# Performance work log

Measured on AMD Instinct MI355X. Metric: run time of the kernel, lower is better.

## Reference

```python
import jax, jax.numpy as jnp
import numpy as np

N_AGENTS = 32
UNIT_DIM = 32
STATE_DIM = 1200
N_HEAD = 8
EMBED = 64
KEY_HID = 2 * EMBED
HYPER = 256
V_HID = 4 * EMBED
ATTEND_REG_COEF = 0.001
BS, T = 128, 32


def setup_inputs() -> dict:
    key = jax.random.key(0)
    ks = jax.random.split(key, 12)
    def lin(k, shape, fan_in):
        return jax.random.normal(k, shape, jnp.float32) / np.sqrt(fan_in)
    return dict(
        agent_qs=jax.random.normal(ks[0], (BS, T, N_AGENTS), jnp.float32),
        states=jax.random.normal(ks[1], (BS, T, STATE_DIM), jnp.float32),
        actions=jax.random.randint(ks[2], (BS, T, N_AGENTS), 0, 20),
        sel_W1=lin(ks[3], (N_HEAD, HYPER, STATE_DIM), STATE_DIM),
        sel_b1=jnp.zeros((N_HEAD, HYPER), jnp.float32),
        sel_W2=lin(ks[4], (N_HEAD, EMBED, HYPER), HYPER),
        key_W1=lin(ks[5], (N_HEAD, KEY_HID, UNIT_DIM + 1), UNIT_DIM + 1),
        key_b1=jnp.zeros((N_HEAD, KEY_HID), jnp.float32),
        key_W2=lin(ks[6], (N_HEAD, EMBED, KEY_HID), KEY_HID),
        wh_W1=lin(ks[7], (HYPER, STATE_DIM), STATE_DIM),
        wh_b1=jnp.zeros((HYPER,), jnp.float32),
        wh_W2=lin(ks[8], (N_HEAD, HYPER), HYPER),
        wh_b2=jnp.zeros((N_HEAD,), jnp.float32),
        v_W1=lin(ks[9], (V_HID, STATE_DIM), STATE_DIM),
        v_b1=jnp.zeros((V_HID,), jnp.float32),
        v_W2=lin(ks[10], (1, V_HID), V_HID),
        v_b2=jnp.zeros((1,), jnp.float32),
    )


def reference(agent_qs, states, actions, sel_W1, sel_b1, sel_W2, key_W1, key_b1, key_W2,
              wh_W1, wh_b1, wh_W2, wh_b2, v_W1, v_b1, v_W2, v_b2):
    bs = agent_qs.shape[0]
    s = states.reshape(-1, STATE_DIM)                       # (B, S), B = bs*T
    B = s.shape[0]
    units = s[:, :UNIT_DIM * N_AGENTS].reshape(B, N_AGENTS, UNIT_DIM)  # (B, A, U)
    q = agent_qs.reshape(B, N_AGENTS)                       # (B, A)
    # nonlinear=True: append each agent's q to its unit features
    units = jnp.concatenate([units, q[:, :, None]], axis=2)  # (B, A, U+1)
    a = actions.reshape(B, N_AGENTS)
    # selector hypernets (all heads batched): (B, H, E)
    h1 = jax.nn.relu(jnp.einsum('bs,hes->bhe', s, sel_W1) + sel_b1[None])
    sel = jnp.einsum('bhe,hde->bhd', h1, sel_W2)
    # key hypernets (all heads x all agents batched): (B, H, A, E)
    k1 = jax.nn.relu(jnp.einsum('bau,hku->bhak', units, key_W1) + key_b1[None, :, None, :])
    keys = jnp.einsum('bhak,hdk->bhad', k1, key_W2)
    logits = jnp.einsum('bhd,bhad->bha', sel, keys)          # unscaled, used for regularizer
    scaled = logits / np.sqrt(EMBED)
    scaled = jnp.where(a[:, None, :] == 0, -99999999.0, scaled)  # mask_dead
    w = jax.nn.softmax(scaled, axis=2)                       # (B, H, A)
    head_q = jnp.einsum('ba,bha->bh', q, w)                  # (B, H)
    # weighted_head + state_bias
    wh = jnp.abs(jax.nn.relu(s @ wh_W1.T + wh_b1) @ wh_W2.T + wh_b2)  # (B, H)
    v = (jax.nn.relu(s @ v_W1.T + v_b1) @ v_W2.T + v_b2)[:, 0]        # (B,)
    y = (wh * head_q).sum(axis=1) + v
    q_tot = y.reshape(bs, -1, 1)
    # sum over heads of per-head mean of squared (unscaled) logits
    attend_mag_regs = ATTEND_REG_COEF * (logits ** 2).mean(axis=(0, 2)).sum()
    # per-head entropy: sum over agents, mean over batch
    head_entropies = -(jnp.log(w + 1e-8) * w).sum(axis=2).mean(axis=0)  # (H,)
    return q_tot, attend_mag_regs, head_entropies
```

## Files before the change

kernel.cpp:

```cpp
#include <hip/hip_runtime.h>

#define B_TOT 4096
#define SDIM  1200
#define KPAD  1216
#define NA    32
#define NH    8
#define EMB   64
#define KHID  128
#define HYP   256
#define NSEL  2048
#define NTOT  2560

#define WS_H1BF 0
#define WS_MBF  (WS_H1BF + (size_t)B_TOT * NTOT / 2)
#define WS_LG   (WS_MBF  + (size_t)B_TOT * NH * KHID / 2)
#define WS_PART (WS_LG   + (size_t)B_TOT * NH * NA)
#define WS_P2   (WS_PART + (size_t)B_TOT * 16)
#define WS_ABF  (WS_P2   + (size_t)32 * 16)
#define WS_WBF  (WS_ABF  + (size_t)B_TOT * KPAD / 2)
#define WS_KW32 (WS_WBF  + (size_t)NTOT * KPAD / 2)
#define WS_B2   (WS_KW32 + (size_t)1024 * 32 / 2)
#define WS_M2T  (WS_B2   + (size_t)1024 * 32 / 2)

#define CVT_A_BLK 4864
#define CVT_W_BLK 3040

typedef __attribute__((ext_vector_type(8))) short short8v;
typedef __attribute__((ext_vector_type(4))) float floatx4;

#define GLL16(gsrc, ldst) __builtin_amdgcn_global_load_lds( \
    (const __attribute__((address_space(1))) unsigned int*)(gsrc), \
    (__attribute__((address_space(3))) unsigned int*)(ldst), 16, 0, 0)

__device__ __forceinline__ ushort f2bf(float x) {
    unsigned u = __builtin_bit_cast(unsigned, x);
    unsigned r = (u + 0x7FFFu + ((u >> 16) & 1u)) >> 16;
    return (ushort)r;
}
__device__ __forceinline__ float bf2f(ushort u) {
    unsigned x = ((unsigned)u) << 16;
    return __builtin_bit_cast(float, x);
}

__global__ __launch_bounds__(256) void k_cvt_all(
    const float* __restrict__ states, const float* __restrict__ sel_W1,
    const float* __restrict__ wh_W1, const float* __restrict__ v_W1,
    const float* __restrict__ key_W1, const float* __restrict__ key_b1,
    ushort* __restrict__ Abf, ushort* __restrict__ Wbf,
    ushort* __restrict__ kw32, ushort* __restrict__ b2bf)
{
    const int gb = blockIdx.x;
    if (gb < CVT_A_BLK) {
        const size_t g = (size_t)gb * 256 + threadIdx.x;
        const int row = (int)(g / (KPAD / 4));
        const int c4  = (int)(g % (KPAD / 4)) * 4;
        ushort4 o = {0, 0, 0, 0};
        if (c4 < SDIM) {
            float4 v = *(const float4*)(states + (size_t)row * SDIM + c4);
            o.x = f2bf(v.x); o.y = f2bf(v.y); o.z = f2bf(v.z); o.w = f2bf(v.w);
        }
        *(ushort4*)(Abf + (size_t)row * KPAD + c4) = o;
    } else if (gb < CVT_A_BLK + CVT_W_BLK) {
        const size_t g = (size_t)(gb - CVT_A_BLK) * 256 + threadIdx.x;
        const int row = (int)(g / (KPAD / 4));
        const int c4  = (int)(g % (KPAD / 4)) * 4;
        const float* src = (row < NSEL)       ? (sel_W1 + (size_t)row * SDIM)
                         : (row < NSEL + HYP) ? (wh_W1 + (size_t)(row - NSEL) * SDIM)
                                              : (v_W1  + (size_t)(row - NSEL - HYP) * SDIM);
        ushort4 o = {0, 0, 0, 0};
        if (c4 < SDIM) {
            float4 v = *(const float4*)(src + c4);
            o.x = f2bf(v.x); o.y = f2bf(v.y); o.z = f2bf(v.z); o.w = f2bf(v.w);
        }
        *(ushort4*)(Wbf + (size_t)row * KPAD + c4) = o;
    } else {
        const int row = (gb - CVT_A_BLK - CVT_W_BLK) * 256 + threadIdx.x;
        if (row >= 1024) return;
        const float* srcr = key_W1 + (size_t)row * 33;
        ushort o[32];
        #pragma unroll
        for (int u = 0; u < 32; ++u) o[u] = f2bf(srcr[u]);
        #pragma unroll
        for (int c = 0; c < 4; ++c)
            *(short8v*)(kw32 + (size_t)row * 32 + c * 8) = *(short8v*)&o[c * 8];
        ushort o2[32] = {};
        o2[0] = f2bf(srcr[32]);
        o2[1] = f2bf(key_b1[row]);
        #pragma unroll
        for (int c = 0; c < 4; ++c)
            *(short8v*)(b2bf + (size_t)row * 32 + c * 8) = *(short8v*)&o2[c * 8];
    }
}

__global__ __launch_bounds__(256) void k_m2(
    const float* __restrict__ sel_W2, const float* __restrict__ key_W2,
    ushort* __restrict__ M2T)
{
    __shared__ float ssel[EMB * HYP];
    __shared__ float skey[EMB][8];
    const int t  = threadIdx.x;
    const int h  = blockIdx.x;
    const int k0 = blockIdx.y * 8;

    const float4* sw = (const float4*)(sel_W2 + (size_t)h * EMB * HYP);
    #pragma unroll
    for (int j = 0; j < 16; ++j)
        ((float4*)ssel)[j * 256 + t] = sw[j * 256 + t];
    if (t < EMB) {
        #pragma unroll
        for (int kk = 0; kk < 8; ++kk)
            skey[t][kk] = key_W2[((size_t)h * EMB + t) * KHID + k0 + kk];
    }
    __syncthreads();

    const int e = t;
    float acc[8] = {};
    for (int d = 0; d < EMB; ++d) {
        const float sv = ssel[d * HYP + e];
        #pragma unroll
        for (int kk = 0; kk < 8; ++kk)
            acc[kk] = fmaf(sv, skey[d][kk], acc[kk]);
    }
    #pragma unroll
    for (int kk = 0; kk < 8; ++kk)
        M2T[((size_t)h * KHID + k0 + kk) * HYP + e] = f2bf(acc[kk]);
}

#define BKG 64
__global__ __launch_bounds__(256) void k_gemm1_mfma(
    const ushort* __restrict__ Abf, const ushort* __restrict__ Wbf,
    const float* __restrict__ sel_b1, const float* __restrict__ wh_b1,
    const float* __restrict__ v_b1, ushort* __restrict__ h1bf)
{
    __shared__ ushort As[128 * BKG];
    __shared__ ushort Bs[128 * BKG];
    const int tid = threadIdx.x;
    const int l   = tid & 63;
    const int w   = tid >> 6;
    const int wM  = w >> 1, wN = w & 1;
    const int arow0 = blockIdx.y * 128;
    const int nrow0 = blockIdx.x * 128;

    const int srow   = tid >> 3;
    const int schunk = tid & 7;
    const int scol   = (schunk ^ (srow & 7)) * 8;
    const ushort* gA = Abf + (size_t)(arow0 + srow) * KPAD + scol;
    const ushort* gB = Wbf + (size_t)(nrow0 + srow) * KPAD + scol;
    ushort* lA = &As[tid * 8];
    ushort* lB = &Bs[tid * 8];

    floatx4 acc[4][4] = {};

    for (int k0 = 0; k0 < KPAD; k0 += BKG) {
        #pragma unroll
        for (int c = 0; c < 4; ++c) {
            GLL16(gA + (size_t)(c * 32) * KPAD + k0, lA + c * 2048);
            GLL16(gB + (size_t)(c * 32) * KPAD + k0, lB + c * 2048);
        }
        __syncthreads();

        #pragma unroll
        for (int kk = 0; kk < 2; ++kk) {
            const int ch = kk * 4 + (l >> 4);
            short8v av[4], bv[4];
            #pragma unroll
            for (int mi = 0; mi < 4; ++mi) {
                const int row = wM * 64 + mi * 16 + (l & 15);
                av[mi] = *(const short8v*)&As[row * BKG + (ch ^ (row & 7)) * 8];
            }
            #pragma unroll
            for (int ni = 0; ni < 4; ++ni) {
                const int row = wN * 64 + ni * 16 + (l & 15);
                bv[ni] = *(const short8v*)&Bs[row * BKG + (ch ^ (row & 7)) * 8];
            }
            #pragma unroll
            for (int mi = 0; mi < 4; ++mi)
                #pragma unroll
                for (int ni = 0; ni < 4; ++ni)
                    acc[mi][ni] = __builtin_amdgcn_mfma_f32_16x16x32_bf16(
                        av[mi], bv[ni], acc[mi][ni], 0, 0, 0);
        }
        __syncthreads();
    }

    float bias_n[4];
    #pragma unroll
    for (int ni = 0; ni < 4; ++ni) {
        const int col = nrow0 + wN * 64 + ni * 16 + (l & 15);
        bias_n[ni] = (col < NSEL)       ? sel_b1[col]
                   : (col < NSEL + HYP) ? wh_b1[col - NSEL]
                                        : v_b1[col - NSEL - HYP];
    }
    #pragma unroll
    for (int mi = 0; mi < 4; ++mi) {
        const int row = arow0 + wM * 64 + mi * 16 + (l >> 4) * 4;
        #pragma unroll
        for (int ni = 0; ni < 4; ++ni) {
            const int col = nrow0 + wN * 64 + ni * 16 + (l & 15);
            #pragma unroll
            for (int r = 0; r < 4; ++r)
                h1bf[(size_t)(row + r) * NTOT + col] =
                    f2bf(fmaxf(acc[mi][ni][r] + bias_n[ni], 0.f));
        }
    }
}

#define BK 32
__global__ __launch_bounds__(256) void k_m_mfma(
    const ushort* __restrict__ h1bf, const ushort* __restrict__ M2T,
    ushort* __restrict__ m_out)
{
    __shared__ ushort As[2][64 * BK];
    __shared__ ushort Bs[2][128 * BK];
    const int tid = threadIdx.x;
    const int l   = tid & 63;
    const int w   = tid >> 6;
    const int wM  = w >> 1, wN = w & 1;
    const int h     = blockIdx.x;
    const int brow0 = blockIdx.y * 64;

    const int srow = tid >> 2;
    const int skof = (tid & 3) * 8;
    const ushort* gA = h1bf + (size_t)(brow0 + srow) * NTOT + h * HYP + skof;
    const ushort* gB = M2T + ((size_t)h * KHID + srow) * HYP + skof;

#define STAGE_M(BUF, KK) do { \
    GLL16(gA + (KK), &As[BUF][srow * BK + skof]); \
    GLL16(gB + (KK), &Bs[BUF][srow * BK + skof]); \
    GLL16(gB + (size_t)64 * HYP + (KK), &Bs[BUF][(64 + srow) * BK + skof]); \
} while (0)

    floatx4 acc[2][4] = {};

    STAGE_M(0, 0);
    __syncthreads();
    int cur = 0;
    for (int k0 = 0; k0 < HYP; k0 += BK) {
        if (k0 + BK < HYP) STAGE_M(cur ^ 1, k0 + BK);

        const int kch = (l >> 4) * 8;
        short8v av[2], bv[4];
        #pragma unroll
        for (int mi = 0; mi < 2; ++mi)
            av[mi] = *(const short8v*)&As[cur][(wM * 32 + mi * 16 + (l & 15)) * BK + kch];
        #pragma unroll
        for (int ni = 0; ni < 4; ++ni)
            bv[ni] = *(const short8v*)&Bs[cur][(wN * 64 + ni * 16 + (l & 15)) * BK + kch];
        #pragma unroll
        for (int mi = 0; mi < 2; ++mi)
            #pragma unroll
            for (int ni = 0; ni < 4; ++ni)
                acc[mi][ni] = __builtin_amdgcn_mfma_f32_16x16x32_bf16(
                    av[mi], bv[ni], acc[mi][ni], 0, 0, 0);
        __syncthreads();
        cur ^= 1;
    }

    #pragma unroll
    for (int mi = 0; mi < 2; ++mi) {
        const int row = brow0 + wM * 32 + mi * 16 + (l >> 4) * 4;
        #pragma unroll
        for (int ni = 0; ni < 4; ++ni) {
            const int col = wN * 64 + ni * 16 + (l & 15);
            #pragma unroll
            for (int r = 0; r < 4; ++r)
                m_out[(((size_t)(row + r) * NH + h) * 16 + (col & 15)) * 8 + (col >> 4)]
                    = f2bf(acc[mi][ni][r]);
        }
    }
}

__global__ __launch_bounds__(256) void k_logits_mfma(
    const ushort* __restrict__ Abf, const ushort* __restrict__ KW32,
    const ushort* __restrict__ B2bf, const float* __restrict__ agent_qs,
    const ushort* __restrict__ mT, float* __restrict__ logits)
{
    const int tid = threadIdx.x;
    const int l   = tid & 63;
    const int w   = tid >> 6;
    const int b   = blockIdx.x * 4 + w;
    const int chunk0 = ((l >> 4) == 0);

    short8v av[2], a2[2];
    #pragma unroll
    for (int mi = 0; mi < 2; ++mi) {
        const int a = mi * 16 + (l & 15);
        av[mi] = *(const short8v*)(
            Abf + (size_t)b * KPAD + a * 32 + (l >> 4) * 8);
        const ushort qb = chunk0 ? f2bf(agent_qs[(size_t)b * NA + a]) : 0;
        short8v t = {};
        t[0] = (short)qb;
        t[1] = (short)(chunk0 ? 0x3F80 : 0);
        a2[mi] = t;
    }

    for (int h = 0; h < NH; ++h) {
        short8v bv[8], bv2[8];
        #pragma unroll
        for (int ni = 0; ni < 8; ++ni) {
            const int k = ni * 16 + (l & 15);
            bv[ni]  = *(const short8v*)(
                KW32 + ((size_t)h * KHID + k) * 32 + (l >> 4) * 8);
            bv2[ni] = *(const short8v*)(
                B2bf + ((size_t)h * KHID + k) * 32 + (l >> 4) * 8);
        }
        short8v mv = *(const short8v*)(
            mT + (((size_t)b * NH + h) * 16 + (l & 15)) * 8);
        float mr[8];
        #pragma unroll
        for (int ni = 0; ni < 8; ++ni) mr[ni] = bf2f((ushort)mv[ni]);

        floatx4 acc[2][8] = {};
        __builtin_amdgcn_s_setprio(1);
        #pragma unroll
        for (int mi = 0; mi < 2; ++mi)
            #pragma unroll
            for (int ni = 0; ni < 8; ++ni) {
                acc[mi][ni] = __builtin_amdgcn_mfma_f32_16x16x32_bf16(
                    av[mi], bv[ni], acc[mi][ni], 0, 0, 0);
                acc[mi][ni] = __builtin_amdgcn_mfma_f32_16x16x32_bf16(
                    a2[mi], bv2[ni], acc[mi][ni], 0, 0, 0);
            }
        __builtin_amdgcn_s_setprio(0);

        #pragma unroll
        for (int mi = 0; mi < 2; ++mi) {
            float s0 = 0.f, s1 = 0.f, s2 = 0.f, s3 = 0.f;
            #pragma unroll
            for (int ni = 0; ni < 8; ++ni) {
                const float mv2 = mr[ni];
                s0 = fmaf(fmaxf(acc[mi][ni][0], 0.f), mv2, s0);
                s1 = fmaf(fmaxf(acc[mi][ni][1], 0.f), mv2, s1);
                s2 = fmaf(fmaxf(acc[mi][ni][2], 0.f), mv2, s2);
                s3 = fmaf(fmaxf(acc[mi][ni][3], 0.f), mv2, s3);
            }
            #pragma unroll
            for (int off = 8; off >= 1; off >>= 1) {
                s0 += __shfl_xor(s0, off);
                s1 += __shfl_xor(s1, off);
                s2 += __shfl_xor(s2, off);
                s3 += __shfl_xor(s3, off);
            }
            if ((l & 15) == 0) {
                float4 o = {s0, s1, s2, s3};
                *(float4*)(logits + ((size_t)b * NH + h) * NA
                           + mi * 16 + (l >> 4) * 4) = o;
            }
        }
    }
}

__global__ __launch_bounds__(256) void k_softmax(
    const float* __restrict__ logits, const float* __restrict__ agent_qs,
    const int* __restrict__ actions, const ushort* __restrict__ h1bf,
    const float* __restrict__ wh_W2, const float* __restrict__ wh_b2,
    const float* __restrict__ v_W2, const float* __restrict__ v_b2,
    float* __restrict__ out, float* __restrict__ part)
{
    __shared__ float qs[NA];
    __shared__ int   act_s[NA];
    __shared__ float whs[NH];
    __shared__ float hq[NH];
    __shared__ float vred[4];
    const int b = blockIdx.x, t = threadIdx.x;
    if (t < NA) {
        qs[t]    = agent_qs[(size_t)b * NA + t];
        act_s[t] = actions[(size_t)b * NA + t];
    }
    const int h = t >> 5, a = t & 31;
    {
        float acc = 0.f;
        #pragma unroll
        for (int j = 0; j < 8; ++j) {
            const int e = a + 32 * j;
            acc = fmaf(bf2f(h1bf[(size_t)b * NTOT + NSEL + e]),
                       wh_W2[h * HYP + e], acc);
        }
        #pragma unroll
        for (int off = 16; off >= 1; off >>= 1) acc += __shfl_xor(acc, off, 32);
        if (a == 0) whs[h] = fabsf(acc + wh_b2[h]);
    }
    {
        float acc = bf2f(h1bf[(size_t)b * NTOT + NSEL + HYP + t]) * v_W2[t];
        #pragma unroll
        for (int off = 32; off >= 1; off >>= 1) acc += __shfl_xor(acc, off);
        if ((t & 63) == 0) vred[t >> 6] = acc;
    }
    __syncthreads();

    const float lg = logits[((size_t)b * NH + h) * NA + a];
    float sc = (act_s[a] == 0) ? -99999999.0f : lg * 0.125f;

    float mx = sc;
    #pragma unroll
    for (int off = 16; off >= 1; off >>= 1) mx = fmaxf(mx, __shfl_xor(mx, off, 32));
    const float e = expf(sc - mx);
    float sum = e;
    #pragma unroll
    for (int off = 16; off >= 1; off >>= 1) sum += __shfl_xor(sum, off, 32);
    const float wgt = e / sum;

    float r_sq  = lg * lg;
    float r_hq  = qs[a] * wgt;
    float r_ent = -wgt * logf(wgt + 1e-8f);
    #pragma unroll
    for (int off = 16; off >= 1; off >>= 1) {
        r_sq  += __shfl_xor(r_sq,  off, 32);
        r_hq  += __shfl_xor(r_hq,  off, 32);
        r_ent += __shfl_xor(r_ent, off, 32);
    }
    if (a == 0) {
        hq[h] = r_hq;
        part[(size_t)b * 16 + h]     = r_sq;
        part[(size_t)b * 16 + 8 + h] = r_ent;
    }
    __syncthreads();
    if (t == 0) {
        float y = vred[0] + vred[1] + vred[2] + vred[3] + v_b2[0];
        #pragma unroll
        for (int i = 0; i < NH; ++i) y = fmaf(whs[i], hq[i], y);
        out[b] = y;
    }
}

__global__ __launch_bounds__(256) void k_final_s1(
    const float* __restrict__ part, float* __restrict__ part2)
{
    __shared__ float red[16][17];
    const int t = threadIdx.x;
    const int c = t & 15, rl = t >> 4;
    const int rbase = blockIdx.x * 128 + rl;
    float v0 = 0.f, v1 = 0.f, v2 = 0.f, v3 = 0.f;
    #pragma unroll
    for (int j = 0; j < 8; j += 4) {
        v0 += part[(size_t)(rbase + (j + 0) * 16) * 16 + c];
        v1 += part[(size_t)(rbase + (j + 1) * 16) * 16 + c];
        v2 += part[(size_t)(rbase + (j + 2) * 16) * 16 + c];
        v3 += part[(size_t)(rbase + (j + 3) * 16) * 16 + c];
    }
    red[rl][c] = (v0 + v1) + (v2 + v3);
    __syncthreads();
    if (t < 16) {
        float s = 0.f;
        #pragma unroll
        for (int i = 0; i < 16; ++i) s += red[i][t];
        part2[blockIdx.x * 16 + t] = s;
    }
}

__global__ __launch_bounds__(256) void k_final_s2(
    const float* __restrict__ part2, float* __restrict__ out)
{
    __shared__ float red[16][17];
    __shared__ float tot[16];
    const int t = threadIdx.x;
    {
        const int g = t >> 4, c = t & 15;
        red[g][c] = part2[t] + part2[t + 256];
    }
    __syncthreads();
    if (t < 16) {
        float s = 0.f;
        #pragma unroll
        for (int i = 0; i < 16; ++i) s += red[i][t];
        tot[t] = s;
    }
    __syncthreads();
    if (t == 0) {
        float s = 0.f;
        #pragma unroll
        for (int i = 0; i < 8; ++i) s += tot[i];
        out[B_TOT] = 0.001f * (s / (float)((size_t)B_TOT * NA));
    }
    if (t >= 8 && t < 16)
        out[B_TOT + 1 + (t - 8)] = tot[t] / (float)B_TOT;
}

extern "C" void kernel_launch(void* const* d_in, const int* in_sizes, int n_in,
                              void* d_out, int out_size, void* d_ws, size_t ws_size,
                              hipStream_t stream) {
    (void)in_sizes; (void)n_in; (void)out_size; (void)ws_size;
    const float* agent_qs = (const float*)d_in[0];
    const float* states   = (const float*)d_in[1];
    const int*   actions  = (const int*)d_in[2];
    const float* sel_W1   = (const float*)d_in[3];
    const float* sel_b1   = (const float*)d_in[4];
    const float* sel_W2   = (const float*)d_in[5];
    const float* key_W1   = (const float*)d_in[6];
    const float* key_b1   = (const float*)d_in[7];
    const float* key_W2   = (const float*)d_in[8];
    const float* wh_W1    = (const float*)d_in[9];
    const float* wh_b1    = (const float*)d_in[10];
    const float* wh_W2    = (const float*)d_in[11];
    const float* wh_b2    = (const float*)d_in[12];
    const float* v_W1     = (const float*)d_in[13];
    const float* v_b1     = (const float*)d_in[14];
    const float* v_W2     = (const float*)d_in[15];
    const float* v_b2     = (const float*)d_in[16];

    float* out = (float*)d_out;
    float* ws  = (float*)d_ws;
    ushort* h1bf  = (ushort*)(ws + WS_H1BF);
    ushort* m_buf = (ushort*)(ws + WS_MBF);
    float* lg_buf = ws + WS_LG;
    float* part   = ws + WS_PART;
    float* part2  = ws + WS_P2;
    ushort* Abf   = (ushort*)(ws + WS_ABF);
    ushort* Wbf   = (ushort*)(ws + WS_WBF);
    ushort* KW32  = (ushort*)(ws + WS_KW32);
    ushort* B2bf  = (ushort*)(ws + WS_B2);
    ushort* M2T   = (ushort*)(ws + WS_M2T);

    k_cvt_all<<<CVT_A_BLK + CVT_W_BLK + 4, 256, 0, stream>>>(
        states, sel_W1, wh_W1, v_W1, key_W1, key_b1, Abf, Wbf, KW32, B2bf);
    k_m2<<<dim3(NH, KHID / 8), 256, 0, stream>>>(sel_W2, key_W2, M2T);
    k_gemm1_mfma<<<dim3(NTOT / 128, B_TOT / 128), 256, 0, stream>>>(
        Abf, Wbf, sel_b1, wh_b1, v_b1, h1bf);
    k_m_mfma<<<dim3(NH, B_TOT / 64), 256, 0, stream>>>(h1bf, M2T, m_buf);
    k_logits_mfma<<<dim3(B_TOT / 4), 256, 0, stream>>>(
        Abf, KW32, B2bf, agent_qs, m_buf, lg_buf);
    k_softmax<<<dim3(B_TOT), 256, 0, stream>>>(
        lg_buf, agent_qs, actions, h1bf, wh_W2, wh_b2, v_W2, v_b2, out, part);
    k_final_s1<<<32, 256, 0, stream>>>(part, part2);
    k_final_s2<<<1, 256, 0, stream>>>(part2, out);
}
```

Baseline: 115.3 us.

## Stage key weights in LDS and pack bias/q-weight into compact buffer

The logits kernel now copies the whole bf16 key_W1 matrix into shared memory once per block, using global_load_lds with an XOR swizzle to avoid bank conflicts. Before, every wave re-read those weights from global memory for each head. The mostly-zero 32-wide B2 rows are replaced by a packed 2-value-per-row buffer, and the sparse MFMA operand is now built in registers. This cuts repeated L2/global traffic, at the cost of about 68KB of LDS per block, which lowers occupancy, plus a block-wide staging barrier.

```diff
diff --git a/kernel.cpp b/kernel.cpp
--- a/kernel.cpp
+++ b/kernel.cpp
@@ -19,8 +19,8 @@
 #define WS_ABF  (WS_P2   + (size_t)32 * 16)
 #define WS_WBF  (WS_ABF  + (size_t)B_TOT * KPAD / 2)
 #define WS_KW32 (WS_WBF  + (size_t)NTOT * KPAD / 2)
-#define WS_B2   (WS_KW32 + (size_t)1024 * 32 / 2)
-#define WS_M2T  (WS_B2   + (size_t)1024 * 32 / 2)
+#define WS_B2P  (WS_KW32 + (size_t)1024 * 32 / 2)
+#define WS_M2T  (WS_B2P  + (size_t)2048 / 2)
 
 #define CVT_A_BLK 4864
 #define CVT_W_BLK 3040
@@ -47,7 +47,7 @@
     const float* __restrict__ wh_W1, const float* __restrict__ v_W1,
     const float* __restrict__ key_W1, const float* __restrict__ key_b1,
     ushort* __restrict__ Abf, ushort* __restrict__ Wbf,
-    ushort* __restrict__ kw32, ushort* __restrict__ b2bf)
+    ushort* __restrict__ kw32, ushort* __restrict__ b2p)
 {
     const int gb = blockIdx.x;
     if (gb < CVT_A_BLK) {
@@ -83,12 +83,10 @@
         #pragma unroll
         for (int c = 0; c < 4; ++c)
             *(short8v*)(kw32 + (size_t)row * 32 + c * 8) = *(short8v*)&o[c * 8];
-        ushort o2[32] = {};
-        o2[0] = f2bf(srcr[32]);
-        o2[1] = f2bf(key_b1[row]);
-        #pragma unroll
-        for (int c = 0; c < 4; ++c)
-            *(short8v*)(b2bf + (size_t)row * 32 + c * 8) = *(short8v*)&o2[c * 8];
+        const int h = row >> 7, k = row & 127;
+        const size_t po = (((size_t)h * 16 + (k & 15)) * 8 + (k >> 4)) * 2;
+        b2p[po]     = f2bf(srcr[32]);
+        b2p[po + 1] = f2bf(key_b1[row]);
     }
 }
 
@@ -272,14 +270,25 @@
 
 __global__ __launch_bounds__(256) void k_logits_mfma(
     const ushort* __restrict__ Abf, const ushort* __restrict__ KW32,
-    const ushort* __restrict__ B2bf, const float* __restrict__ agent_qs,
+    const ushort* __restrict__ B2p, const float* __restrict__ agent_qs,
     const ushort* __restrict__ mT, float* __restrict__ logits)
 {
+    __shared__ ushort Ws[1024 * 32];
+    __shared__ ushort Bp[2048];
     const int tid = threadIdx.x;
     const int l   = tid & 63;
     const int w   = tid >> 6;
     const int b   = blockIdx.x * 4 + w;
     const int chunk0 = ((l >> 4) == 0);
+
+    #pragma unroll
+    for (int i = 0; i < 16; ++i) {
+        const int u = i * 256 + tid;
+        const int row = u >> 2, c = u & 3;
+        GLL16(KW32 + (size_t)row * 32 + (size_t)(c ^ ((row >> 1) & 3)) * 8,
+              &Ws[(size_t)u * 8]);
+    }
+    GLL16(B2p + (size_t)tid * 8, &Bp[(size_t)tid * 8]);
 
     short8v av[2], a2[2];
     #pragma unroll
@@ -293,16 +302,24 @@
         t[1] = (short)(chunk0 ? 0x3F80 : 0);
         a2[mi] = t;
     }
+    __syncthreads();
 
     for (int h = 0; h < NH; ++h) {
+        const int bpo = (h * 16 + (l & 15)) * 16;
+        short8v wb0 = *(const short8v*)&Bp[bpo];
+        short8v wb1 = *(const short8v*)&Bp[bpo + 8];
         short8v bv[8], bv2[8];
         #pragma unroll
         for (int ni = 0; ni < 8; ++ni) {
-            const int k = ni * 16 + (l & 15);
-            bv[ni]  = *(const short8v*)(
-                KW32 + ((size_t)h * KHID + k) * 32 + (l >> 4) * 8);
-            bv2[ni] = *(const short8v*)(
-                B2bf + ((size_t)h * KHID + k) * 32 + (l >> 4) * 8);
+            const int row = h * KHID + ni * 16 + (l & 15);
+            bv[ni] = *(const short8v*)&Ws[(size_t)row * 32
+                        + (size_t)(((l >> 4) ^ ((row >> 1) & 3))) * 8];
+            short8v t = {};
+            if (chunk0) {
+                t[0] = (ni < 4) ? wb0[ni * 2]     : wb1[(ni - 4) * 2];
+                t[1] = (ni < 4) ? wb0[ni * 2 + 1] : wb1[(ni - 4) * 2 + 1];
+            }
+            bv2[ni] = t;
         }
         short8v mv = *(const short8v*)(
             mT + (((size_t)b * NH + h) * 16 + (l & 15)) * 8);
@@ -508,17 +525,17 @@
     ushort* Abf   = (ushort*)(ws + WS_ABF);
     ushort* Wbf   = (ushort*)(ws + WS_WBF);
     ushort* KW32  = (ushort*)(ws + WS_KW32);
-    ushort* B2bf  = (ushort*)(ws + WS_B2);
+    ushort* B2p   = (ushort*)(ws + WS_B2P);
     ushort* M2T   = (ushort*)(ws + WS_M2T);
 
     k_cvt_all<<<CVT_A_BLK + CVT_W_BLK + 4, 256, 0, stream>>>(
-        states, sel_W1, wh_W1, v_W1, key_W1, key_b1, Abf, Wbf, KW32, B2bf);
+        states, sel_W1, wh_W1, v_W1, key_W1, key_b1, Abf, Wbf, KW32, B2p);
     k_m2<<<dim3(NH, KHID / 8), 256, 0, stream>>>(sel_W2, key_W2, M2T);
     k_gemm1_mfma<<<dim3(NTOT / 128, B_TOT / 128), 256, 0, stream>>>(
         Abf, Wbf, sel_b1, wh_b1, v_b1, h1bf);
     k_m_mfma<<<dim3(NH, B_TOT / 64), 256, 0, stream>>>(h1bf, M2T, m_buf);
     k_logits_mfma<<<dim3(B_TOT / 4), 256, 0, stream>>>(
-        Abf, KW32, B2bf, agent_qs, m_buf, lg_buf);
+        Abf, KW32, B2p, agent_qs, m_buf, lg_buf);
     k_softmax<<<dim3(B_TOT), 256, 0, stream>>>(
         lg_buf, agent_qs, actions, h1bf, wh_W2, wh_b2, v_W2, v_b2, out, part);
     k_final_s1<<<32, 256, 0, stream>>>(part, part2);
```

Measured after the change: 114.5 us. About the same (-0.7%).
